# Optimization experiments

Measured on AMD Instinct MI355X. Metric: run time of the kernel, lower is better.

Reference implementation:

```python
import jax, jax.numpy as jnp
import numpy as np

N = 50000
E = 600000
IN_DIM = 128
D = 32          # out_dim per head
H = 4           # heads
M = 3           # num metapaths
HID = 128       # semantic attention hidden
NEG_SLOPE = 0.2


def setup_inputs() -> dict:
    key = jax.random.key(0)
    ks = jax.random.split(key, 12)
    x = jax.random.normal(ks[0], (N, IN_DIM), dtype=jnp.float32)
    mp_edge_index = jax.random.randint(ks[1], (M, 2, E), 0, N, dtype=jnp.int64)
    s = 1.0 / np.sqrt(IN_DIM)
    W = jax.random.normal(ks[2], (M, IN_DIM, H * D), dtype=jnp.float32) * s
    att_src = jax.random.normal(ks[3], (M, H, D), dtype=jnp.float32) * (1.0 / np.sqrt(D))
    att_dst = jax.random.normal(ks[4], (M, H, D), dtype=jnp.float32) * (1.0 / np.sqrt(D))
    bias = jnp.zeros((M, H * D), dtype=jnp.float32)
    ln_gamma = jnp.ones((H * D,), dtype=jnp.float32)
    ln_beta = jnp.zeros((H * D,), dtype=jnp.float32)
    sem_W1 = jax.random.normal(ks[5], (H * D, HID), dtype=jnp.float32) * (1.0 / np.sqrt(H * D))
    sem_b1 = jnp.zeros((HID,), dtype=jnp.float32)
    sem_W2 = jax.random.normal(ks[6], (HID, 1), dtype=jnp.float32) * (1.0 / np.sqrt(HID))
    return dict(x=x, mp_edge_index=mp_edge_index, W=W, att_src=att_src,
                att_dst=att_dst, bias=bias, ln_gamma=ln_gamma, ln_beta=ln_beta,
                sem_W1=sem_W1, sem_b1=sem_b1, sem_W2=sem_W2)


def _gat_conv(x, edge_index, W_m, a_src, a_dst, b_m):
    # PyG GATConv (add_self_loops=True, concat=True). x: [N, F_in]
    n = x.shape[0]
    h = (x @ W_m).reshape(n, H, D)                       # [N, H, D]
    loops = jnp.arange(n, dtype=edge_index.dtype)
    src = jnp.concatenate([edge_index[0], loops])        # [E+N]
    dst = jnp.concatenate([edge_index[1], loops])
    alpha_s = jnp.einsum('nhd,hd->nh', h, a_src)         # [N, H]
    alpha_d = jnp.einsum('nhd,hd->nh', h, a_dst)
    e = jax.nn.leaky_relu(alpha_s[src] + alpha_d[dst], NEG_SLOPE)  # [E+N, H]
    # segment softmax over edges grouped by destination node
    e_max = jax.ops.segment_max(e, dst, num_segments=n)
    e = jnp.exp(e - e_max[dst])
    denom = jax.ops.segment_sum(e, dst, num_segments=n)
    alpha = e / (denom[dst] + 1e-16)                     # [E+N, H]
    msg = h[src] * alpha[:, :, None]                     # [E+N, H, D]
    out = jax.ops.segment_sum(msg, dst, num_segments=n)  # [N, H, D]
    return out.reshape(n, H * D) + b_m


def _layer_norm(y, gamma, beta):
    mu = y.mean(-1, keepdims=True)
    var = y.var(-1, keepdims=True)
    return (y - mu) * jax.lax.rsqrt(var + 1e-5) * gamma + beta


def reference(x, mp_edge_index, W, att_src, att_dst, bias, ln_gamma, ln_beta,
              sem_W1, sem_b1, sem_W2):
    embs = []
    for i in range(M):
        emb = _gat_conv(x, mp_edge_index[i], W[i], att_src[i], att_dst[i], bias[i])
        emb = jax.nn.elu(_layer_norm(emb, ln_gamma, ln_beta))
        embs.append(emb)
    z = jnp.stack(embs, axis=1)                          # [N, M, H*D]
    # semantic attention
    w = (jnp.tanh(z @ sem_W1 + sem_b1) @ sem_W2).mean(0)  # [M, 1]
    beta = jax.nn.softmax(w, axis=0)                      # [M, 1]
    out_emb = (beta[None, :, :] * z).sum(1)               # [N, H*D]
    att_mp = beta.squeeze()                               # [M]
    return out_emb, att_mp
```

## Files before the change

### kernel.cpp

```cpp
#include <hip/hip_runtime.h>
#include <hip/hip_bf16.h>

#define N_NODES 50000
#define N_EDGES 600000
#define NMETA   3
#define LTOT (NMETA * N_NODES)
#define SPAN_SHIFT 9
#define NBUCK 98
#define BCAP 8192
#define NCHUNK 147
#define LOG2E 1.4426950408889634f

typedef unsigned short u16;
typedef short bf16x8 __attribute__((ext_vector_type(8)));
typedef float f32x4 __attribute__((ext_vector_type(4)));

__device__ __forceinline__ float bf2f(u16 v) {
    union { unsigned int u; float f; } x; x.u = ((unsigned int)v) << 16; return x.f;
}
__device__ __forceinline__ u16 f2bf(float f) {
    return __hip_bfloat16_raw(__float2bfloat16(f)).x;
}

__global__ __launch_bounds__(256) void k_build1(
    const int* __restrict__ ei, int* __restrict__ gcnt,
    unsigned long long* __restrict__ pairs,
    const float* __restrict__ W, const float* __restrict__ W1,
    u16* __restrict__ WT, u16* __restrict__ W1T)
{
    const int bid = blockIdx.x;
    const int t = threadIdx.x;
    if (bid >= NMETA * NCHUNK) {
        int idx = (bid - NMETA * NCHUNK) * 256 + t;
        if (idx < NMETA * 16384) {
            int m = idx >> 14, r = idx & 16383;
            int col = r >> 7, k = r & 127;
            WT[idx] = f2bf(W[(m << 14) + k * 128 + col]);
        } else {
            int r = idx - NMETA * 16384;
            int col = r >> 7, k = r & 127;
            W1T[r] = f2bf(W1[k * 128 + col]);
        }
        return;
    }
    const int m = bid / NCHUNK;
    const int e0 = (bid % NCHUNK) * 4096;
    __shared__ int cnt[NBUCK];
    __shared__ int gbase[NBUCK];
    if (t < NBUCK) cnt[t] = 0;
    __syncthreads();
    const int* srcp = ei + (size_t)m * 2 * N_EDGES;
    const int* dstp = srcp + N_EDGES;
    int sa[16], da[16], sl[16];
    #pragma unroll
    for (int j = 0; j < 16; ++j) {
        int e = e0 + j * 256 + t;
        if (e < N_EDGES) {
            int s = srcp[e], d = dstp[e];
            if ((unsigned)s >= N_NODES) s = 0;
            if ((unsigned)d >= N_NODES) d = 0;
            sa[j] = s; da[j] = d;
            sl[j] = atomicAdd(&cnt[d >> SPAN_SHIFT], 1);
        } else sl[j] = -1;
    }
    __syncthreads();
    if (t < NBUCK) gbase[t] = atomicAdd(&gcnt[m * NBUCK + t], cnt[t]);
    __syncthreads();
    #pragma unroll
    for (int j = 0; j < 16; ++j) {
        if (sl[j] < 0) continue;
        int b = da[j] >> SPAN_SHIFT;
        int pos = gbase[b] + sl[j];
        if (pos < BCAP)
            pairs[(size_t)(m * NBUCK + b) * BCAP + pos] =
                ((unsigned long long)(da[j] & 511) << 32) | (unsigned)(sa[j] * 128);
    }
}

__global__ __launch_bounds__(256) void k_build2(
    const int* __restrict__ gcnt, const unsigned long long* __restrict__ pairs,
    int* __restrict__ row_start, int* __restrict__ row_end, int* __restrict__ eidx,
    const float* __restrict__ x, const u16* __restrict__ WT,
    const float* __restrict__ att_src, const float* __restrict__ att_dst,
    u16* __restrict__ h, float* __restrict__ alpha_s, float* __restrict__ alpha_d)
{
    const int bid = blockIdx.x;
    const int t = threadIdx.x;
    if (bid < NMETA * NBUCK) {
        const int m = bid / NBUCK, b = bid % NBUCK;
        __shared__ int cnt[512];
        __shared__ int off[512];
        __shared__ int wsum[4];
        int nb = gcnt[m * NBUCK + b]; if (nb > BCAP) nb = BCAP;
        const int base = (m * NBUCK + b) * BCAP;
        cnt[t] = 0; cnt[t + 256] = 0;
        __syncthreads();
        for (int e = t; e < nb; e += 256) {
            int dl = (int)(pairs[(size_t)base + e] >> 32);
            atomicAdd(&cnt[dl], 1);
        }
        __syncthreads();
        int v0 = cnt[2 * t], v1 = cnt[2 * t + 1];
        int s = v0 + v1;
        int lane = t & 63, wv = t >> 6;
        int incl = s;
        #pragma unroll
        for (int o = 1; o < 64; o <<= 1) {
            int u = __shfl_up(incl, o);
            if (lane >= o) incl += u;
        }
        if (lane == 63) wsum[wv] = incl;
        __syncthreads();
        int woff = 0;
        for (int i = 0; i < wv; ++i) woff += wsum[i];
        int ex = woff + incl - s;
        off[2 * t] = ex;
        off[2 * t + 1] = ex + v0;
        __syncthreads();
        const int node0 = b << SPAN_SHIFT;
        for (int i = t; i < 512; i += 256) {
            int n = node0 + i;
            if (n < N_NODES) {
                int st = base + off[i];
                row_start[m * N_NODES + n] = st;
                row_end[m * N_NODES + n]   = st + cnt[i];
            }
        }
        __syncthreads();
        for (int e = t; e < nb; e += 256) {
            unsigned long long p = pairs[(size_t)base + e];
            int dl = (int)(p >> 32);
            int pos = atomicAdd(&off[dl], 1);
            eidx[(size_t)base + pos] = (dl << 23) | (int)(unsigned)p;
        }
        return;
    }
    const int g = bid - NMETA * NBUCK;
    const int bx = g % 782, m = g / 782;
    const int wv = t >> 6, lane = t & 63;
    const int row0 = (bx * 4 + wv) * 16;
    if (row0 >= N_NODES) return;
    const int lhi = lane >> 4, llo = lane & 15;
    const float* xrow = x + (size_t)(row0 + llo) * 128 + lhi * 8;
    bf16x8 a[4];
    #pragma unroll
    for (int ks = 0; ks < 4; ++ks) {
        float4 f0 = *(const float4*)(xrow + ks * 32);
        float4 f1 = *(const float4*)(xrow + ks * 32 + 4);
        bf16x8 av;
        av[0] = f2bf(f0.x); av[1] = f2bf(f0.y); av[2] = f2bf(f0.z); av[3] = f2bf(f0.w);
        av[4] = f2bf(f1.x); av[5] = f2bf(f1.y); av[6] = f2bf(f1.z); av[7] = f2bf(f1.w);
        a[ks] = av;
    }
    const u16* wbase = WT + (size_t)m * 16384 + (size_t)llo * 128 + lhi * 8;
    u16* hm = h + ((size_t)m * N_NODES + row0) * 128;
    float sp[4][4], dp[4][4];
    #pragma unroll
    for (int i = 0; i < 4; ++i)
        #pragma unroll
        for (int r = 0; r < 4; ++r) { sp[i][r] = 0.f; dp[i][r] = 0.f; }
    #pragma unroll
    for (int cf = 0; cf < 8; ++cf) {
        f32x4 acc = {0.f, 0.f, 0.f, 0.f};
        const u16* wp = wbase + cf * 16 * 128;
        #pragma unroll
        for (int ks = 0; ks < 4; ++ks) {
            bf16x8 b = *(const bf16x8*)(wp + ks * 32);
            acc = __builtin_amdgcn_mfma_f32_16x16x32_bf16(a[ks], b, acc, 0, 0, 0);
        }
        const int col = cf * 16 + llo;
        const int hh = cf >> 1;
        const float as = att_src[m * 128 + col];
        const float adv = att_dst[m * 128 + col];
        #pragma unroll
        for (int r = 0; r < 4; ++r) {
            hm[(size_t)(lhi * 4 + r) * 128 + col] = f2bf(acc[r]);
            sp[hh][r] += acc[r] * as;
            dp[hh][r] += acc[r] * adv;
        }
    }
    #pragma unroll
    for (int o = 1; o <= 8; o <<= 1) {
        #pragma unroll
        for (int i = 0; i < 4; ++i)
            #pragma unroll
            for (int r = 0; r < 4; ++r) {
                sp[i][r] += __shfl_xor(sp[i][r], o);
                dp[i][r] += __shfl_xor(dp[i][r], o);
            }
    }
    if (llo == 0) {
        #pragma unroll
        for (int r = 0; r < 4; ++r) {
            int n = row0 + lhi * 4 + r;
            f32x4 vs = {sp[0][r] * LOG2E, sp[1][r] * LOG2E, sp[2][r] * LOG2E, sp[3][r] * LOG2E};
            f32x4 vd = {dp[0][r] * LOG2E, dp[1][r] * LOG2E, dp[2][r] * LOG2E, dp[3][r] * LOG2E};
            *(f32x4*)(alpha_s + ((size_t)m * N_NODES + n) * 4) = vs;
            *(f32x4*)(alpha_d + ((size_t)m * N_NODES + n) * 4) = vd;
        }
    }
}

__global__ __launch_bounds__(256) void k_ew(
    const int* __restrict__ gcnt, int* __restrict__ eidx,
    const float* __restrict__ alpha_s, const float* __restrict__ alpha_d,
    u16* __restrict__ ew)
{
    const int bucket = blockIdx.x;
    const int m = bucket / NBUCK, b = bucket % NBUCK;
    int nb = gcnt[bucket]; if (nb > BCAP) nb = BCAP;
    const int base = bucket * BCAP;
    const int node0 = b << SPAN_SHIFT;
    const float* as_m = alpha_s + (size_t)m * N_NODES * 4;
    const float* ad_m = alpha_d + (size_t)m * N_NODES * 4;
    for (int i = threadIdx.x; i < nb; i += 256) {
        int v = eidx[base + i];
        int src128 = v & 0x7FFFFF;
        int dl = (unsigned)v >> 23;
        f32x4 as4 = *(const f32x4*)(as_m + (src128 >> 5));
        f32x4 ad4 = *(const f32x4*)(ad_m + (size_t)(node0 + dl) * 4);
        ushort4 e4;
        u16* ep = (u16*)&e4;
        #pragma unroll
        for (int k = 0; k < 4; ++k) {
            float pre = as4[k] + ad4[k];
            pre = fmaxf(pre, 0.2f * pre);
            ep[k] = f2bf(exp2f(pre));
        }
        *(ushort4*)(ew + (size_t)(base + i) * 4) = e4;
        eidx[base + i] = src128 * 2;
    }
}

__global__ __launch_bounds__(256) void k_gather(
    const int* __restrict__ row_start, const int* __restrict__ row_end,
    const int* __restrict__ eidx, const u16* __restrict__ ew,
    const float* __restrict__ alpha_s, const float* __restrict__ alpha_d,
    const u16* __restrict__ h,
    const float* __restrict__ bias, const float* __restrict__ gamma,
    const float* __restrict__ lbeta,
    u16* __restrict__ z)
{
    long long w = ((long long)blockIdx.x * blockDim.x + threadIdx.x) >> 6;
    if (w >= (long long)LTOT) return;
    int m = (int)(w / N_NODES), n = (int)(w % N_NODES);
    int lane = threadIdx.x & 63, hh = lane >> 4;
    const char* h_m = (const char*)(h + (size_t)m * N_NODES * 128);
    const int lb = lane * 4;
    const float* as_m = alpha_s + (size_t)m * N_NODES * 4;
    const float* ad_m = alpha_d + (size_t)m * N_NODES * 4;
    float pre = as_m[n * 4 + hh] + ad_m[n * 4 + hh];
    pre = fmaxf(pre, 0.2f * pre);
    float ev = exp2f(pre);
    float esum = ev;
    ushort2 hv = *(const ushort2*)(h_m + (size_t)n * 256 + lb);
    float acc0 = ev * bf2f(hv.x), acc1 = ev * bf2f(hv.y);
    int p = row_start[m * N_NODES + n];
    const int end = row_end[m * N_NODES + n];
    for (; p + 3 < end; p += 4) {
        int o1 = eidx[p], o2 = eidx[p + 1], o3 = eidx[p + 2], o4 = eidx[p + 3];
        float e1 = bf2f(ew[(size_t)p * 4 + hh]);
        float e2 = bf2f(ew[(size_t)p * 4 + 4 + hh]);
        float e3 = bf2f(ew[(size_t)p * 4 + 8 + hh]);
        float e4 = bf2f(ew[(size_t)p * 4 + 12 + hh]);
        ushort2 h1 = *(const ushort2*)(h_m + o1 + lb);
        ushort2 h2 = *(const ushort2*)(h_m + o2 + lb);
        ushort2 h3 = *(const ushort2*)(h_m + o3 + lb);
        ushort2 h4 = *(const ushort2*)(h_m + o4 + lb);
        esum += (e1 + e2) + (e3 + e4);
        acc0 += e1 * bf2f(h1.x) + e2 * bf2f(h2.x) + e3 * bf2f(h3.x) + e4 * bf2f(h4.x);
        acc1 += e1 * bf2f(h1.y) + e2 * bf2f(h2.y) + e3 * bf2f(h3.y) + e4 * bf2f(h4.y);
    }
    for (; p < end; ++p) {
        int o1 = eidx[p];
        float e1 = bf2f(ew[(size_t)p * 4 + hh]);
        ushort2 h1 = *(const ushort2*)(h_m + o1 + lb);
        esum += e1;
        acc0 += e1 * bf2f(h1.x);
        acc1 += e1 * bf2f(h1.y);
    }
    float rinv = 1.f / (esum + 1e-16f);
    float v0 = acc0 * rinv + bias[m * 128 + lane * 2];
    float v1 = acc1 * rinv + bias[m * 128 + lane * 2 + 1];
    float s1 = v0 + v1, s2 = v0 * v0 + v1 * v1;
    #pragma unroll
    for (int o = 32; o >= 1; o >>= 1) { s1 += __shfl_xor(s1, o); s2 += __shfl_xor(s2, o); }
    float mu = s1 * (1.f / 128.f);
    float var = s2 * (1.f / 128.f) - mu * mu;
    float rs = rsqrtf(var + 1e-5f);
    float o0 = (v0 - mu) * rs * gamma[lane * 2]     + lbeta[lane * 2];
    float o1 = (v1 - mu) * rs * gamma[lane * 2 + 1] + lbeta[lane * 2 + 1];
    o0 = o0 > 0.f ? o0 : (__expf(o0) - 1.f);
    o1 = o1 > 0.f ? o1 : (__expf(o1) - 1.f);
    ushort2 outv; outv.x = f2bf(o0); outv.y = f2bf(o1);
    *(ushort2*)(z + ((size_t)n * NMETA + m) * 128 + lane * 2) = outv;
}

__global__ __launch_bounds__(256) void k_sem(
    const u16* __restrict__ z,
    const u16* __restrict__ W1T,
    const float* __restrict__ b1,
    const float* __restrict__ W2,
    float* __restrict__ wpart)
{
    __shared__ float part[NMETA];
    const int t = threadIdx.x;
    if (t < NMETA) part[t] = 0.f;
    __syncthreads();
    const int wv = t >> 6, lane = t & 63;
    const int row0 = (blockIdx.x * 4 + wv) * 16;
    if (row0 < LTOT) {
        const int lhi = lane >> 4, llo = lane & 15;
        const u16* zrow = z + (size_t)(row0 + llo) * 128 + lhi * 8;
        bf16x8 a[4];
        #pragma unroll
        for (int ks = 0; ks < 4; ++ks) a[ks] = *(const bf16x8*)(zrow + ks * 32);
        const u16* wb = W1T + (size_t)llo * 128 + lhi * 8;
        float rowacc[4] = {0.f, 0.f, 0.f, 0.f};
        #pragma unroll
        for (int cf = 0; cf < 8; ++cf) {
            f32x4 acc = {0.f, 0.f, 0.f, 0.f};
            const u16* wp = wb + cf * 16 * 128;
            #pragma unroll
            for (int ks = 0; ks < 4; ++ks) {
                bf16x8 bb = *(const bf16x8*)(wp + ks * 32);
                acc = __builtin_amdgcn_mfma_f32_16x16x32_bf16(a[ks], bb, acc, 0, 0, 0);
            }
            int col = cf * 16 + llo;
            float b1v = b1[col], w2v = W2[col];
            #pragma unroll
            for (int r = 0; r < 4; ++r)
                rowacc[r] += tanhf(acc[r] + b1v) * w2v;
        }
        #pragma unroll
        for (int o = 1; o <= 8; o <<= 1) {
            #pragma unroll
            for (int r = 0; r < 4; ++r) rowacc[r] += __shfl_xor(rowacc[r], o);
        }
        if (llo == 0) {
            #pragma unroll
            for (int r = 0; r < 4; ++r)
                atomicAdd(&part[(row0 + lhi * 4 + r) % NMETA], rowacc[r]);
        }
    }
    __syncthreads();
    if (t < NMETA) atomicAdd(&wpart[t], part[t]);
}

__global__ void k_beta(const float* __restrict__ wpart, float* __restrict__ betab,
                       float* __restrict__ attout)
{
    if (threadIdx.x == 0 && blockIdx.x == 0) {
        float w0 = wpart[0] * (1.f / N_NODES);
        float w1 = wpart[1] * (1.f / N_NODES);
        float w2 = wpart[2] * (1.f / N_NODES);
        float mx = fmaxf(w0, fmaxf(w1, w2));
        float e0 = __expf(w0 - mx), e1 = __expf(w1 - mx), e2 = __expf(w2 - mx);
        float s = 1.f / (e0 + e1 + e2);
        float b0 = e0 * s, b1 = e1 * s, b2 = e2 * s;
        betab[0] = b0; betab[1] = b1; betab[2] = b2;
        attout[0] = b0; attout[1] = b1; attout[2] = b2;
    }
}

__global__ __launch_bounds__(256) void k_combine(
    const u16* __restrict__ z, const float* __restrict__ betab,
    float* __restrict__ out)
{
    int idx = blockIdx.x * blockDim.x + threadIdx.x;
    if (idx >= N_NODES * 64) return;
    int n = idx >> 6, c2 = (idx & 63) * 2;
    float b0 = betab[0], b1 = betab[1], b2 = betab[2];
    const u16* zp = z + (size_t)n * NMETA * 128 + c2;
    ushort2 a0 = *(const ushort2*)(zp);
    ushort2 a1 = *(const ushort2*)(zp + 128);
    ushort2 a2 = *(const ushort2*)(zp + 256);
    float2 ov;
    ov.x = b0 * bf2f(a0.x) + b1 * bf2f(a1.x) + b2 * bf2f(a2.x);
    ov.y = b0 * bf2f(a0.y) + b1 * bf2f(a1.y) + b2 * bf2f(a2.y);
    *(float2*)(out + (size_t)n * 128 + c2) = ov;
}

extern "C" void kernel_launch(void* const* d_in, const int* in_sizes, int n_in,
                              void* d_out, int out_size, void* d_ws, size_t ws_size,
                              hipStream_t stream) {
    const float* x       = (const float*)d_in[0];
    const int*   ei      = (const int*)d_in[1];
    const float* W       = (const float*)d_in[2];
    const float* att_src = (const float*)d_in[3];
    const float* att_dst = (const float*)d_in[4];
    const float* bias    = (const float*)d_in[5];
    const float* gamma   = (const float*)d_in[6];
    const float* lbeta   = (const float*)d_in[7];
    const float* W1      = (const float*)d_in[8];
    const float* b1      = (const float*)d_in[9];
    const float* W2      = (const float*)d_in[10];

    char* ws = (char*)d_ws;
    size_t off = 0;
    int* gcnt    = (int*)(ws + off);  off += sizeof(int) * 512;
    float* wpart = (float*)(ws + off);
    float* betab = wpart + 8;         off += 64;
    const size_t zero_bytes = off;
    off = (off + 255) & ~(size_t)255;
    int* row_start = (int*)(ws + off); off += sizeof(int) * 150016;
    int* row_end   = (int*)(ws + off); off += sizeof(int) * 150016;
    u16* h      = (u16*)(ws + off);    off += sizeof(u16) * (size_t)NMETA * N_NODES * 128;
    float* alpha_s = (float*)(ws + off); off += sizeof(float) * (size_t)LTOT * 4;
    float* alpha_d = (float*)(ws + off); off += sizeof(float) * (size_t)LTOT * 4;
    u16* WT     = (u16*)(ws + off);    off += sizeof(u16) * (size_t)NMETA * 128 * 128;
    u16* W1T    = (u16*)(ws + off);    off += sizeof(u16) * (size_t)128 * 128;
    int* eidx   = (int*)(ws + off);    off += sizeof(int) * (size_t)NMETA * NBUCK * BCAP;
    u16* ew     = (u16*)(ws + off);    off += sizeof(u16) * (size_t)NMETA * NBUCK * BCAP * 4;
    unsigned long long* pairs = (unsigned long long*)(ws + off);
    u16* z = (u16*)(ws + off);
    off += sizeof(u16) * (size_t)N_NODES * NMETA * 128;
    if (ws_size < off) return;

    hipMemsetAsync(d_ws, 0, zero_bytes, stream);

    k_build1<<<dim3(NMETA * NCHUNK + 256), 256, 0, stream>>>(ei, gcnt, pairs, W, W1, WT, W1T);
    k_build2<<<dim3(NMETA * NBUCK + 782 * NMETA), 256, 0, stream>>>(
        gcnt, pairs, row_start, row_end, eidx,
        x, WT, att_src, att_dst, h, alpha_s, alpha_d);
    k_ew<<<dim3(NMETA * NBUCK), 256, 0, stream>>>(gcnt, eidx, alpha_s, alpha_d, ew);
    k_gather<<<dim3((LTOT + 3) / 4), 256, 0, stream>>>(row_start, row_end, eidx, ew,
                                                       alpha_s, alpha_d, h,
                                                       bias, gamma, lbeta, z);
    k_sem<<<dim3((LTOT / 16 + 3) / 4), 256, 0, stream>>>(z, W1T, b1, W2, wpart);
    k_beta<<<1, 64, 0, stream>>>(wpart, betab, (float*)d_out + (size_t)N_NODES * 128);
    k_combine<<<dim3((N_NODES * 64 + 255) / 256), 256, 0, stream>>>(z, betab, (float*)d_out);
}
```

Before: 287.0 us.

## Compute attention logits from folded W·att in build1 and fuse edge weights into CSR build

Folds att_src/att_dst into W (W·a per head) so alpha_s/alpha_d are computed directly from x in extra k_build1 blocks in fp32. This lets k_build2 compute the bf16 edge exp-weights while scattering edges into CSR, removing the separate k_ew kernel and its re-read of eidx. Rows are padded to multiples of 4 and edge weights are stored in an interleaved 4-edge layout so the gather can use vector int4/uint2 loads. In exchange, k_build1 does a redundant per-block W·att reduction and a CUDA-core dot product, and the padded rows can overflow BCAP, in which case edges are dropped.

```diff
diff --git a/kernel.cpp b/kernel.cpp
--- a/kernel.cpp
+++ b/kernel.cpp
@@ -9,6 +9,7 @@
 #define NBUCK 98
 #define BCAP 8192
 #define NCHUNK 147
+#define NABLK 782
 #define LOG2E 1.4426950408889634f
 
 typedef unsigned short u16;
@@ -17,6 +18,9 @@
 
 __device__ __forceinline__ float bf2f(u16 v) {
     union { unsigned int u; float f; } x; x.u = ((unsigned int)v) << 16; return x.f;
+}
+__device__ __forceinline__ float u2f(unsigned int u) {
+    union { unsigned int u; float f; } x; x.u = u; return x.f;
 }
 __device__ __forceinline__ u16 f2bf(float f) {
     return __hip_bfloat16_raw(__float2bfloat16(f)).x;
@@ -26,10 +30,54 @@
     const int* __restrict__ ei, int* __restrict__ gcnt,
     unsigned long long* __restrict__ pairs,
     const float* __restrict__ W, const float* __restrict__ W1,
-    u16* __restrict__ WT, u16* __restrict__ W1T)
+    u16* __restrict__ WT, u16* __restrict__ W1T,
+    const float* __restrict__ x,
+    const float* __restrict__ att_src, const float* __restrict__ att_dst,
+    float* __restrict__ alpha_s, float* __restrict__ alpha_d)
 {
     const int bid = blockIdx.x;
     const int t = threadIdx.x;
+    if (bid >= NMETA * NCHUNK + 256) {
+        __shared__ float va[6][128][4];
+        __shared__ float xl[64][129];
+        const int row0 = (bid - (NMETA * NCHUNK + 256)) * 64;
+        for (int idx = t; idx < 3072; idx += 256) {
+            int v = idx >> 9, r = idx & 511, k = r >> 2, hh = r & 3;
+            int m = v >> 1;
+            const float* att = ((v & 1) ? att_dst : att_src) + m * 128 + hh * 32;
+            const float* wp = W + (size_t)m * 16384 + k * 128 + hh * 32;
+            float s = 0.f;
+            #pragma unroll
+            for (int d = 0; d < 32; ++d) s += wp[d] * att[d];
+            va[v][k][hh] = s * LOG2E;
+        }
+        for (int i = t; i < 64 * 32; i += 256) {
+            int r = i >> 5, q = i & 31;
+            int n = row0 + r;
+            float4 vx = make_float4(0.f, 0.f, 0.f, 0.f);
+            if (n < N_NODES) vx = ((const float4*)(x + (size_t)n * 128))[q];
+            xl[r][q * 4 + 0] = vx.x; xl[r][q * 4 + 1] = vx.y;
+            xl[r][q * 4 + 2] = vx.z; xl[r][q * 4 + 3] = vx.w;
+        }
+        __syncthreads();
+        const int r = t & 63;
+        const int n = row0 + r;
+        for (int v = t >> 6; v < 6; v += 4) {
+            float a0 = 0.f, a1 = 0.f, a2 = 0.f, a3 = 0.f;
+            for (int k = 0; k < 128; ++k) {
+                float xk = xl[r][k];
+                float4 vv = *(const float4*)&va[v][k][0];
+                a0 += xk * vv.x; a1 += xk * vv.y; a2 += xk * vv.z; a3 += xk * vv.w;
+            }
+            if (n < N_NODES) {
+                int m = v >> 1;
+                float* dst = ((v & 1) ? alpha_d : alpha_s) + ((size_t)m * N_NODES + n) * 4;
+                f32x4 o = {a0, a1, a2, a3};
+                *(f32x4*)dst = o;
+            }
+        }
+        return;
+    }
     if (bid >= NMETA * NCHUNK) {
         int idx = (bid - NMETA * NCHUNK) * 256 + t;
         if (idx < NMETA * 16384) {
@@ -80,9 +128,10 @@
 __global__ __launch_bounds__(256) void k_build2(
     const int* __restrict__ gcnt, const unsigned long long* __restrict__ pairs,
     int* __restrict__ row_start, int* __restrict__ row_end, int* __restrict__ eidx,
+    u16* __restrict__ ew,
+    const float* __restrict__ alpha_s, const float* __restrict__ alpha_d,
     const float* __restrict__ x, const u16* __restrict__ WT,
-    const float* __restrict__ att_src, const float* __restrict__ att_dst,
-    u16* __restrict__ h, float* __restrict__ alpha_s, float* __restrict__ alpha_d)
+    u16* __restrict__ h)
 {
     const int bid = blockIdx.x;
     const int t = threadIdx.x;
@@ -100,8 +149,9 @@
             atomicAdd(&cnt[dl], 1);
         }
         __syncthreads();
-        int v0 = cnt[2 * t], v1 = cnt[2 * t + 1];
-        int s = v0 + v1;
+        int c0 = cnt[2 * t], c1 = cnt[2 * t + 1];
+        int v0p = (c0 + 3) & ~3, v1p = (c1 + 3) & ~3;
+        int s = v0p + v1p;
         int lane = t & 63, wv = t >> 6;
         int incl = s;
         #pragma unroll
@@ -115,7 +165,7 @@
         for (int i = 0; i < wv; ++i) woff += wsum[i];
         int ex = woff + incl - s;
         off[2 * t] = ex;
-        off[2 * t + 1] = ex + v0;
+        off[2 * t + 1] = ex + v0p;
         __syncthreads();
         const int node0 = b << SPAN_SHIFT;
         for (int i = t; i < 512; i += 256) {
@@ -127,16 +177,30 @@
             }
         }
         __syncthreads();
+        const float* as_m = alpha_s + (size_t)m * N_NODES * 4;
+        const float* ad_m = alpha_d + (size_t)m * N_NODES * 4;
         for (int e = t; e < nb; e += 256) {
             unsigned long long p = pairs[(size_t)base + e];
             int dl = (int)(p >> 32);
+            int src128 = (int)(unsigned)p;
             int pos = atomicAdd(&off[dl], 1);
-            eidx[(size_t)base + pos] = (dl << 23) | (int)(unsigned)p;
+            int slot = base + pos;
+            if (pos >= BCAP) continue;
+            eidx[slot] = src128 * 2;
+            f32x4 as4 = *(const f32x4*)(as_m + (src128 >> 5));
+            f32x4 ad4 = *(const f32x4*)(ad_m + (size_t)(node0 + dl) * 4);
+            u16* ewp = ew + (size_t)(slot >> 2) * 16 + (slot & 3);
+            #pragma unroll
+            for (int k = 0; k < 4; ++k) {
+                float pre = as4[k] + ad4[k];
+                pre = fmaxf(pre, 0.2f * pre);
+                ewp[k * 4] = f2bf(exp2f(pre));
+            }
         }
         return;
     }
     const int g = bid - NMETA * NBUCK;
-    const int bx = g % 782, m = g / 782;
+    const int bx = g % NABLK, m = g / NABLK;
     const int wv = t >> 6, lane = t & 63;
     const int row0 = (bx * 4 + wv) * 16;
     if (row0 >= N_NODES) return;
@@ -154,81 +218,19 @@
     }
     const u16* wbase = WT + (size_t)m * 16384 + (size_t)llo * 128 + lhi * 8;
     u16* hm = h + ((size_t)m * N_NODES + row0) * 128;
-    float sp[4][4], dp[4][4];
-    #pragma unroll
-    for (int i = 0; i < 4; ++i)
-        #pragma unroll
-        for (int r = 0; r < 4; ++r) { sp[i][r] = 0.f; dp[i][r] = 0.f; }
     #pragma unroll
     for (int cf = 0; cf < 8; ++cf) {
         f32x4 acc = {0.f, 0.f, 0.f, 0.f};
         const u16* wp = wbase + cf * 16 * 128;
         #pragma unroll
         for (int ks = 0; ks < 4; ++ks) {
-            bf16x8 b = *(const bf16x8*)(wp + ks * 32);
-            acc = __builtin_amdgcn_mfma_f32_16x16x32_bf16(a[ks], b, acc, 0, 0, 0);
+            bf16x8 bb = *(const bf16x8*)(wp + ks * 32);
+            acc = __builtin_amdgcn_mfma_f32_16x16x32_bf16(a[ks], bb, acc, 0, 0, 0);
         }
         const int col = cf * 16 + llo;
-        const int hh = cf >> 1;
-        const float as = att_src[m * 128 + col];
-        const float adv = att_dst[m * 128 + col];
-        #pragma unroll
-        for (int r = 0; r < 4; ++r) {
+        #pragma unroll
+        for (int r = 0; r < 4; ++r)
             hm[(size_t)(lhi * 4 + r) * 128 + col] = f2bf(acc[r]);
-            sp[hh][r] += acc[r] * as;
-            dp[hh][r] += acc[r] * adv;
-        }
-    }
-    #pragma unroll
-    for (int o = 1; o <= 8; o <<= 1) {
-        #pragma unroll
-        for (int i = 0; i < 4; ++i)
-            #pragma unroll
-            for (int r = 0; r < 4; ++r) {
-                sp[i][r] += __shfl_xor(sp[i][r], o);
-                dp[i][r] += __shfl_xor(dp[i][r], o);
-            }
-    }
-    if (llo == 0) {
-        #pragma unroll
-        for (int r = 0; r < 4; ++r) {
-            int n = row0 + lhi * 4 + r;
-            f32x4 vs = {sp[0][r] * LOG2E, sp[1][r] * LOG2E, sp[2][r] * LOG2E, sp[3][r] * LOG2E};
-            f32x4 vd = {dp[0][r] * LOG2E, dp[1][r] * LOG2E, dp[2][r] * LOG2E, dp[3][r] * LOG2E};
-            *(f32x4*)(alpha_s + ((size_t)m * N_NODES + n) * 4) = vs;
-            *(f32x4*)(alpha_d + ((size_t)m * N_NODES + n) * 4) = vd;
-        }
-    }
-}
-
-__global__ __launch_bounds__(256) void k_ew(
-    const int* __restrict__ gcnt, int* __restrict__ eidx,
-    const float* __restrict__ alpha_s, const float* __restrict__ alpha_d,
-    u16* __restrict__ ew)
-{
-    const int bucket = blockIdx.x;
-    const int m = bucket / NBUCK, b = bucket % NBUCK;
-    int nb = gcnt[bucket]; if (nb > BCAP) nb = BCAP;
-    const int base = bucket * BCAP;
-    const int node0 = b << SPAN_SHIFT;
-    const float* as_m = alpha_s + (size_t)m * N_NODES * 4;
-    const float* ad_m = alpha_d + (size_t)m * N_NODES * 4;
-    for (int i = threadIdx.x; i < nb; i += 256) {
-        int v = eidx[base + i];
-        int src128 = v & 0x7FFFFF;
-        int dl = (unsigned)v >> 23;
-        f32x4 as4 = *(const f32x4*)(as_m + (src128 >> 5));
-        f32x4 ad4 = *(const f32x4*)(ad_m + (size_t)(node0 + dl) * 4);
-        ushort4 e4;
-        u16* ep = (u16*)&e4;
-        #pragma unroll
-        for (int k = 0; k < 4; ++k) {
-            float pre = as4[k] + ad4[k];
-            pre = fmaxf(pre, 0.2f * pre);
-            ep[k] = f2bf(exp2f(pre));
-        }
-        *(ushort4*)(ew + (size_t)(base + i) * 4) = e4;
-        eidx[base + i] = src128 * 2;
     }
 }
 
@@ -246,6 +248,7 @@
     int m = (int)(w / N_NODES), n = (int)(w % N_NODES);
     int lane = threadIdx.x & 63, hh = lane >> 4;
     const char* h_m = (const char*)(h + (size_t)m * N_NODES * 128);
+    const char* ewb = (const char*)ew;
     const int lb = lane * 4;
     const float* as_m = alpha_s + (size_t)m * N_NODES * 4;
     const float* ad_m = alpha_d + (size_t)m * N_NODES * 4;
@@ -258,22 +261,21 @@
     int p = row_start[m * N_NODES + n];
     const int end = row_end[m * N_NODES + n];
     for (; p + 3 < end; p += 4) {
-        int o1 = eidx[p], o2 = eidx[p + 1], o3 = eidx[p + 2], o4 = eidx[p + 3];
-        float e1 = bf2f(ew[(size_t)p * 4 + hh]);
-        float e2 = bf2f(ew[(size_t)p * 4 + 4 + hh]);
-        float e3 = bf2f(ew[(size_t)p * 4 + 8 + hh]);
-        float e4 = bf2f(ew[(size_t)p * 4 + 12 + hh]);
-        ushort2 h1 = *(const ushort2*)(h_m + o1 + lb);
-        ushort2 h2 = *(const ushort2*)(h_m + o2 + lb);
-        ushort2 h3 = *(const ushort2*)(h_m + o3 + lb);
-        ushort2 h4 = *(const ushort2*)(h_m + o4 + lb);
+        int4 o4 = *(const int4*)(eidx + p);
+        uint2 ewv = *(const uint2*)(ewb + (size_t)(p + hh) * 8);
+        float e1 = u2f(ewv.x << 16), e2 = u2f(ewv.x & 0xffff0000u);
+        float e3 = u2f(ewv.y << 16), e4 = u2f(ewv.y & 0xffff0000u);
+        ushort2 h1 = *(const ushort2*)(h_m + o4.x + lb);
+        ushort2 h2 = *(const ushort2*)(h_m + o4.y + lb);
+        ushort2 h3 = *(const ushort2*)(h_m + o4.z + lb);
+        ushort2 h4 = *(const ushort2*)(h_m + o4.w + lb);
         esum += (e1 + e2) + (e3 + e4);
         acc0 += e1 * bf2f(h1.x) + e2 * bf2f(h2.x) + e3 * bf2f(h3.x) + e4 * bf2f(h4.x);
         acc1 += e1 * bf2f(h1.y) + e2 * bf2f(h2.y) + e3 * bf2f(h3.y) + e4 * bf2f(h4.y);
     }
     for (; p < end; ++p) {
         int o1 = eidx[p];
-        float e1 = bf2f(ew[(size_t)p * 4 + hh]);
+        float e1 = bf2f(*(const u16*)(ewb + (size_t)((p & ~3) + hh) * 8 + (p & 3) * 2));
         ushort2 h1 = *(const ushort2*)(h_m + o1 + lb);
         esum += e1;
         acc0 += e1 * bf2f(h1.x);
@@ -297,10 +299,8 @@
 }
 
 __global__ __launch_bounds__(256) void k_sem(
-    const u16* __restrict__ z,
-    const u16* __restrict__ W1T,
-    const float* __restrict__ b1,
-    const float* __restrict__ W2,
+    const u16* __restrict__ z, const u16* __restrict__ W1T,
+    const float* __restrict__ b1, const float* __restrict__ W2,
     float* __restrict__ wpart)
 {
     __shared__ float part[NMETA];
@@ -419,11 +419,10 @@
 
     hipMemsetAsync(d_ws, 0, zero_bytes, stream);
 
-    k_build1<<<dim3(NMETA * NCHUNK + 256), 256, 0, stream>>>(ei, gcnt, pairs, W, W1, WT, W1T);
-    k_build2<<<dim3(NMETA * NBUCK + 782 * NMETA), 256, 0, stream>>>(
-        gcnt, pairs, row_start, row_end, eidx,
-        x, WT, att_src, att_dst, h, alpha_s, alpha_d);
-    k_ew<<<dim3(NMETA * NBUCK), 256, 0, stream>>>(gcnt, eidx, alpha_s, alpha_d, ew);
+    k_build1<<<dim3(NMETA * NCHUNK + 256 + NABLK), 256, 0, stream>>>(
+        ei, gcnt, pairs, W, W1, WT, W1T, x, att_src, att_dst, alpha_s, alpha_d);
+    k_build2<<<dim3(NMETA * NBUCK + NABLK * NMETA), 256, 0, stream>>>(
+        gcnt, pairs, row_start, row_end, eidx, ew, alpha_s, alpha_d, x, WT, h);
     k_gather<<<dim3((LTOT + 3) / 4), 256, 0, stream>>>(row_start, row_end, eidx, ew,
                                                        alpha_s, alpha_d, h,
                                                        bias, gamma, lbeta, z);
```

New measurement: 396.9 us. 1.38x slower.

## Pad per-node edge rows to multiples of four and interleave edge weights

Applied to the files above, without the earlier changes.

Each destination node's CSR row is padded to a multiple of four slots, and the padding entries are zeroed. Edge weights are stored in a blocked layout, four edges per head group, so the gather loop can load four indices as one int4 and four weights as one uint2. k_ew becomes a grid-stride loop over all slots with a fixed 2048 blocks, replacing one block per bucket. This adds padded slots, extra zeroing work and more bucket-capacity pressure. Rows that are not a multiple of four can still fall through to the scalar tail.

```diff
diff --git a/kernel.cpp b/kernel.cpp
--- a/kernel.cpp
+++ b/kernel.cpp
@@ -9,6 +9,8 @@
 #define NBUCK 98
 #define BCAP 8192
 #define NCHUNK 147
+#define NABLK 782
+#define NSLOT (NMETA * NBUCK * BCAP)
 #define LOG2E 1.4426950408889634f
 
 typedef unsigned short u16;
@@ -17,6 +19,9 @@
 
 __device__ __forceinline__ float bf2f(u16 v) {
     union { unsigned int u; float f; } x; x.u = ((unsigned int)v) << 16; return x.f;
+}
+__device__ __forceinline__ float u2f(unsigned int u) {
+    union { unsigned int u; float f; } x; x.u = u; return x.f;
 }
 __device__ __forceinline__ u16 f2bf(float f) {
     return __hip_bfloat16_raw(__float2bfloat16(f)).x;
@@ -80,6 +85,7 @@
 __global__ __launch_bounds__(256) void k_build2(
     const int* __restrict__ gcnt, const unsigned long long* __restrict__ pairs,
     int* __restrict__ row_start, int* __restrict__ row_end, int* __restrict__ eidx,
+    int* __restrict__ ptot,
     const float* __restrict__ x, const u16* __restrict__ WT,
     const float* __restrict__ att_src, const float* __restrict__ att_dst,
     u16* __restrict__ h, float* __restrict__ alpha_s, float* __restrict__ alpha_d)
@@ -100,8 +106,9 @@
             atomicAdd(&cnt[dl], 1);
         }
         __syncthreads();
-        int v0 = cnt[2 * t], v1 = cnt[2 * t + 1];
-        int s = v0 + v1;
+        int c0 = cnt[2 * t], c1 = cnt[2 * t + 1];
+        int v0p = (c0 + 3) & ~3, v1p = (c1 + 3) & ~3;
+        int s = v0p + v1p;
         int lane = t & 63, wv = t >> 6;
         int incl = s;
         #pragma unroll
@@ -115,7 +122,13 @@
         for (int i = 0; i < wv; ++i) woff += wsum[i];
         int ex = woff + incl - s;
         off[2 * t] = ex;
-        off[2 * t + 1] = ex + v0;
+        off[2 * t + 1] = ex + v0p;
+        if (t == 255) {
+            int tot = ex + v0p + v1p;
+            ptot[m * NBUCK + b] = tot < BCAP ? tot : BCAP;
+        }
+        for (int q = ex + c0; q < ex + v0p && q < BCAP; ++q) eidx[base + q] = 0;
+        for (int q = ex + v0p + c1; q < ex + v0p + v1p && q < BCAP; ++q) eidx[base + q] = 0;
         __syncthreads();
         const int node0 = b << SPAN_SHIFT;
         for (int i = t; i < 512; i += 256) {
@@ -131,12 +144,13 @@
             unsigned long long p = pairs[(size_t)base + e];
             int dl = (int)(p >> 32);
             int pos = atomicAdd(&off[dl], 1);
-            eidx[(size_t)base + pos] = (dl << 23) | (int)(unsigned)p;
+            if (pos >= BCAP) continue;
+            eidx[base + pos] = (dl << 23) | (int)(unsigned)p;
         }
         return;
     }
     const int g = bid - NMETA * NBUCK;
-    const int bx = g % 782, m = g / 782;
+    const int bx = g % NABLK, m = g / NABLK;
     const int wv = t >> 6, lane = t & 63;
     const int row0 = (bx * 4 + wv) * 16;
     if (row0 >= N_NODES) return;
@@ -165,8 +179,8 @@
         const u16* wp = wbase + cf * 16 * 128;
         #pragma unroll
         for (int ks = 0; ks < 4; ++ks) {
-            bf16x8 b = *(const bf16x8*)(wp + ks * 32);
-            acc = __builtin_amdgcn_mfma_f32_16x16x32_bf16(a[ks], b, acc, 0, 0, 0);
+            bf16x8 bb = *(const bf16x8*)(wp + ks * 32);
+            acc = __builtin_amdgcn_mfma_f32_16x16x32_bf16(a[ks], bb, acc, 0, 0, 0);
         }
         const int col = cf * 16 + llo;
         const int hh = cf >> 1;
@@ -202,33 +216,31 @@
 }
 
 __global__ __launch_bounds__(256) void k_ew(
-    const int* __restrict__ gcnt, int* __restrict__ eidx,
+    const int* __restrict__ ptot, int* __restrict__ eidx,
     const float* __restrict__ alpha_s, const float* __restrict__ alpha_d,
     u16* __restrict__ ew)
 {
-    const int bucket = blockIdx.x;
-    const int m = bucket / NBUCK, b = bucket % NBUCK;
-    int nb = gcnt[bucket]; if (nb > BCAP) nb = BCAP;
-    const int base = bucket * BCAP;
-    const int node0 = b << SPAN_SHIFT;
-    const float* as_m = alpha_s + (size_t)m * N_NODES * 4;
-    const float* ad_m = alpha_d + (size_t)m * N_NODES * 4;
-    for (int i = threadIdx.x; i < nb; i += 256) {
-        int v = eidx[base + i];
+    for (int sidx = blockIdx.x * 256 + threadIdx.x; sidx < NSLOT; sidx += gridDim.x * 256) {
+        const int bucket = sidx >> 13;
+        const int i = sidx & (BCAP - 1);
+        if (i >= ptot[bucket]) continue;
+        const int m = bucket / NBUCK, b = bucket % NBUCK;
+        const int node0 = b << SPAN_SHIFT;
+        int v = eidx[sidx];
         int src128 = v & 0x7FFFFF;
         int dl = (unsigned)v >> 23;
+        const float* as_m = alpha_s + (size_t)m * N_NODES * 4;
+        const float* ad_m = alpha_d + (size_t)m * N_NODES * 4;
         f32x4 as4 = *(const f32x4*)(as_m + (src128 >> 5));
         f32x4 ad4 = *(const f32x4*)(ad_m + (size_t)(node0 + dl) * 4);
-        ushort4 e4;
-        u16* ep = (u16*)&e4;
+        u16* ewp = ew + (size_t)(sidx >> 2) * 16 + (sidx & 3);
         #pragma unroll
         for (int k = 0; k < 4; ++k) {
             float pre = as4[k] + ad4[k];
             pre = fmaxf(pre, 0.2f * pre);
-            ep[k] = f2bf(exp2f(pre));
-        }
-        *(ushort4*)(ew + (size_t)(base + i) * 4) = e4;
-        eidx[base + i] = src128 * 2;
+            ewp[k * 4] = f2bf(exp2f(pre));
+        }
+        eidx[sidx] = src128 * 2;
     }
 }
 
@@ -246,6 +258,7 @@
     int m = (int)(w / N_NODES), n = (int)(w % N_NODES);
     int lane = threadIdx.x & 63, hh = lane >> 4;
     const char* h_m = (const char*)(h + (size_t)m * N_NODES * 128);
+    const char* ewb = (const char*)ew;
     const int lb = lane * 4;
     const float* as_m = alpha_s + (size_t)m * N_NODES * 4;
     const float* ad_m = alpha_d + (size_t)m * N_NODES * 4;
@@ -258,22 +271,21 @@
     int p = row_start[m * N_NODES + n];
     const int end = row_end[m * N_NODES + n];
     for (; p + 3 < end; p += 4) {
-        int o1 = eidx[p], o2 = eidx[p + 1], o3 = eidx[p + 2], o4 = eidx[p + 3];
-        float e1 = bf2f(ew[(size_t)p * 4 + hh]);
-        float e2 = bf2f(ew[(size_t)p * 4 + 4 + hh]);
-        float e3 = bf2f(ew[(size_t)p * 4 + 8 + hh]);
-        float e4 = bf2f(ew[(size_t)p * 4 + 12 + hh]);
-        ushort2 h1 = *(const ushort2*)(h_m + o1 + lb);
-        ushort2 h2 = *(const ushort2*)(h_m + o2 + lb);
-        ushort2 h3 = *(const ushort2*)(h_m + o3 + lb);
-        ushort2 h4 = *(const ushort2*)(h_m + o4 + lb);
+        int4 o4 = *(const int4*)(eidx + p);
+        uint2 ewv = *(const uint2*)(ewb + (size_t)(p + hh) * 8);
+        float e1 = u2f(ewv.x << 16), e2 = u2f(ewv.x & 0xffff0000u);
+        float e3 = u2f(ewv.y << 16), e4 = u2f(ewv.y & 0xffff0000u);
+        ushort2 h1 = *(const ushort2*)(h_m + o4.x + lb);
+        ushort2 h2 = *(const ushort2*)(h_m + o4.y + lb);
+        ushort2 h3 = *(const ushort2*)(h_m + o4.z + lb);
+        ushort2 h4 = *(const ushort2*)(h_m + o4.w + lb);
         esum += (e1 + e2) + (e3 + e4);
         acc0 += e1 * bf2f(h1.x) + e2 * bf2f(h2.x) + e3 * bf2f(h3.x) + e4 * bf2f(h4.x);
         acc1 += e1 * bf2f(h1.y) + e2 * bf2f(h2.y) + e3 * bf2f(h3.y) + e4 * bf2f(h4.y);
     }
     for (; p < end; ++p) {
         int o1 = eidx[p];
-        float e1 = bf2f(ew[(size_t)p * 4 + hh]);
+        float e1 = bf2f(*(const u16*)(ewb + (size_t)((p & ~3) + hh) * 8 + (p & 3) * 2));
         ushort2 h1 = *(const ushort2*)(h_m + o1 + lb);
         esum += e1;
         acc0 += e1 * bf2f(h1.x);
@@ -297,10 +309,8 @@
 }
 
 __global__ __launch_bounds__(256) void k_sem(
-    const u16* __restrict__ z,
-    const u16* __restrict__ W1T,
-    const float* __restrict__ b1,
-    const float* __restrict__ W2,
+    const u16* __restrict__ z, const u16* __restrict__ W1T,
+    const float* __restrict__ b1, const float* __restrict__ W2,
     float* __restrict__ wpart)
 {
     __shared__ float part[NMETA];
@@ -399,6 +409,7 @@
     char* ws = (char*)d_ws;
     size_t off = 0;
     int* gcnt    = (int*)(ws + off);  off += sizeof(int) * 512;
+    int* ptot    = (int*)(ws + off);  off += sizeof(int) * 512;
     float* wpart = (float*)(ws + off);
     float* betab = wpart + 8;         off += 64;
     const size_t zero_bytes = off;
@@ -410,8 +421,8 @@
     float* alpha_d = (float*)(ws + off); off += sizeof(float) * (size_t)LTOT * 4;
     u16* WT     = (u16*)(ws + off);    off += sizeof(u16) * (size_t)NMETA * 128 * 128;
     u16* W1T    = (u16*)(ws + off);    off += sizeof(u16) * (size_t)128 * 128;
-    int* eidx   = (int*)(ws + off);    off += sizeof(int) * (size_t)NMETA * NBUCK * BCAP;
-    u16* ew     = (u16*)(ws + off);    off += sizeof(u16) * (size_t)NMETA * NBUCK * BCAP * 4;
+    int* eidx   = (int*)(ws + off);    off += sizeof(int) * (size_t)NSLOT;
+    u16* ew     = (u16*)(ws + off);    off += sizeof(u16) * (size_t)NSLOT * 4;
     unsigned long long* pairs = (unsigned long long*)(ws + off);
     u16* z = (u16*)(ws + off);
     off += sizeof(u16) * (size_t)N_NODES * NMETA * 128;
@@ -420,10 +431,10 @@
     hipMemsetAsync(d_ws, 0, zero_bytes, stream);
 
     k_build1<<<dim3(NMETA * NCHUNK + 256), 256, 0, stream>>>(ei, gcnt, pairs, W, W1, WT, W1T);
-    k_build2<<<dim3(NMETA * NBUCK + 782 * NMETA), 256, 0, stream>>>(
-        gcnt, pairs, row_start, row_end, eidx,
+    k_build2<<<dim3(NMETA * NBUCK + NABLK * NMETA), 256, 0, stream>>>(
+        gcnt, pairs, row_start, row_end, eidx, ptot,
         x, WT, att_src, att_dst, h, alpha_s, alpha_d);
-    k_ew<<<dim3(NMETA * NBUCK), 256, 0, stream>>>(gcnt, eidx, alpha_s, alpha_d, ew);
+    k_ew<<<dim3(2048), 256, 0, stream>>>(ptot, eidx, alpha_s, alpha_d, ew);
     k_gather<<<dim3((LTOT + 3) / 4), 256, 0, stream>>>(row_start, row_end, eidx, ew,
                                                        alpha_s, alpha_d, h,
                                                        bias, gamma, lbeta, z);
```

Result: faster. 279.8 us (-2.5%).
